# Kernel tuning notes

Hardware: AMD Instinct MI355X
Metric: run time of the kernel (lower is better)

## Reference

```python
import jax, jax.numpy as jnp
import numpy as np
from jax import lax

RANK = 8
ALPHA = 16.0
SCALING = ALPHA / RANK  # 2.0
C_IN, C_OUT, KH, KW = 128, 256, 3, 3


def setup_inputs() -> dict:
    key = jax.random.key(0)
    k1, k2, k3, k4, k5 = jax.random.split(key, 5)
    x = jax.random.normal(k1, (16, C_IN, 64, 64), dtype=jnp.float32)
    W = jax.random.normal(k2, (C_OUT, C_IN, KH, KW), dtype=jnp.float32) * 0.05
    b = jax.random.normal(k3, (C_OUT,), dtype=jnp.float32) * 0.05
    lora_A = jax.random.normal(k4, (RANK, C_IN * KH * KW), dtype=jnp.float32) * 0.02
    lora_B = jax.random.normal(k5, (C_OUT, RANK), dtype=jnp.float32) * 0.02
    return {"x": x, "W": W, "b": b, "lora_A": lora_A, "lora_B": lora_B}


def _conv(x, w, stride=(1, 1), padding=((1, 1), (1, 1))):
    return lax.conv_general_dilated(
        x, w, window_strides=stride, padding=padding,
        dimension_numbers=("NCHW", "OIHW", "NCHW"))


def reference(x, W, b, lora_A, lora_B):
    # Base (frozen) conv: [B, C_out, H, W]
    base_out = _conv(x, W) + b[None, :, None, None]
    # LoRA path. The torch code does im2col -> (BL, C_in*kh*kw) @ A.T @ B.T.
    # Because unfold flattens patches channel-major as (C_in, kh, kw), the
    # identical math is: rank-r conv with A reshaped as [rank, C_in, kh, kw],
    # then a 1x1 mix with B. Same result, no im2col materialization.
    A_k = lora_A.reshape(RANK, C_IN, KH, KW)
    h = _conv(x, A_k)                                   # [B, rank, H, W]
    lora_out = jnp.einsum("brhw,or->bohw", h, lora_B) * SCALING
    return base_out + lora_out
```

## Files before the change

kernel.cpp:

```cpp
#include <hip/hip_runtime.h>
#include <hip/hip_bf16.h>


#define CIN   128
#define COUT  256
#define NBAT  16
#define HPAD  66
#define WPAD  66

typedef __bf16 bf16x8 __attribute__((ext_vector_type(8)));
typedef float f32x4 __attribute__((ext_vector_type(4)));

#define XPAD_ELEMS ((size_t)NBAT * HPAD * WPAD * CIN)
#define XPAD_BYTES (XPAD_ELEMS * 2)
#define WT_ELEMS   ((size_t)9 * COUT * CIN)
#define WS_NEED    (XPAD_BYTES + WT_ELEMS * 2)

typedef __attribute__((address_space(1))) void gvoid;
typedef __attribute__((address_space(3))) void lvoid;

__device__ __forceinline__ void load_lds16(const void* g, void* l) {
    __builtin_amdgcn_global_load_lds((gvoid*)g, (lvoid*)l, 16, 0, 0);
}

__global__ void pad_prep(const float* __restrict__ x, __bf16* __restrict__ xpad,
                         const float* __restrict__ W, const float* __restrict__ lA,
                         const float* __restrict__ lB, __hip_bfloat16* __restrict__ Wt) {
    __shared__ float tile[128][66];
    const int t = threadIdx.x;

    if (blockIdx.x >= 1024) {
        const int idx = (blockIdx.x - 1024) * 256 + t;
        const int c = idx & 127;
        const int o = idx >> 7;
        const int fr    = o & 15;
        const int otile = o >> 4;
        const int cb    = c >> 5;
        const int kc    = (c >> 3) & 3;
        const int j     = c & 7;
        const int lane  = kc * 16 + fr;
        float lb[8];
#pragma unroll
        for (int r = 0; r < 8; ++r) lb[r] = lB[o * 8 + r];
#pragma unroll
        for (int tap = 0; tap < 9; ++tap) {
            float acc = W[(o * 128 + c) * 9 + tap];
            float s = 0.f;
#pragma unroll
            for (int r = 0; r < 8; ++r)
                s += lb[r] * lA[r * 1152 + c * 9 + tap];
            const size_t widx = (((size_t)(tap * 4 + cb) * 16 + otile) * 64 + lane) * 8 + j;
            Wt[widx] = __float2bfloat16(acc + 2.0f * s);
        }
        return;
    }

    const int n = blockIdx.x >> 6;
    const int h = blockIdx.x & 63;
    const float* src = x + (size_t)n * 128 * 4096 + (size_t)h * 64;
#pragma unroll
    for (int i = 0; i < 8; ++i) {
        int g  = i * 256 + t;
        int c  = g >> 4;
        int w4 = (g & 15) * 4;
        const float4 v = *reinterpret_cast<const float4*>(src + (size_t)c * 4096 + w4);
        const int wb = w4 ^ (((c >> 3) & 7) << 2);
        tile[c][wb + 0] = v.x; tile[c][wb + 1] = v.y;
        tile[c][wb + 2] = v.z; tile[c][wb + 3] = v.w;
    }
    __syncthreads();
    __bf16* dst = xpad + ((size_t)(n * 66 + h + 1) * 66 + 1) * 128;
#pragma unroll
    for (int i = 0; i < 4; ++i) {
        int g  = i * 256 + t;
        int w  = g >> 4;
        int c0 = (g & 15) * 8;
        const int swr = ((c0 >> 3) & 7) << 2;
        bf16x8 v;
#pragma unroll
        for (int j = 0; j < 8; ++j) v[j] = (__bf16)tile[c0 + j][w ^ swr];
        *reinterpret_cast<bf16x8*>(dst + (size_t)w * 128 + c0) = v;
    }
    bf16x8 z = {};
    __bf16* rowbase = xpad + (size_t)(n * 66 + h + 1) * 66 * 128;
    if (t < 32) {
        int ww = (t < 16) ? 0 : 65;
        int c0 = (t & 15) * 8;
        *reinterpret_cast<bf16x8*>(rowbase + (size_t)ww * 128 + c0) = z;
    }
    if (h == 0 || h == 63) {
        __bf16* hrow = xpad + (size_t)(n * 66 + (h == 0 ? 0 : 65)) * 66 * 128;
        for (int i = t; i < 66 * 16; i += 256)
            *reinterpret_cast<bf16x8*>(hrow + (size_t)i * 8) = z;
    }
}

__global__ void __launch_bounds__(512, 2) conv_mfma(
    const __bf16* __restrict__ xpad, const __bf16* __restrict__ Wt,
    const float* __restrict__ bias, float* __restrict__ out) {
    __shared__ __align__(16) __bf16 lds[32768];

    const int tid  = threadIdx.x;
    const int wv   = tid >> 6;
    const int lane = tid & 63;

    const int n  = blockIdx.x >> 4;
    const int h0 = (blockIdx.x & 15) << 2;

    const int lrow = lane >> 2;
    const int lswz = (((lane & 3) ^ ((lane >> 3) & 3)) << 3);
    const __bf16* bG[2];
#pragma unroll
    for (int j = 0; j < 2; ++j) {
        const int r0 = j * 128 + wv * 16;
        bG[j] = xpad + (((size_t)(n * 66 + h0 + (r0 >> 6)) * 66 + (r0 & 63) + lrow) * 128) + lswz;
    }

    const int wo   = (wv >> 2) << 7;
    const int wot  = (wv >> 2) << 3;
    const int wpix = (wv & 3) << 6;
    const int fr   = lane & 15;
    const int fphys = (((lane >> 4) ^ ((lane >> 1) & 3)) << 3);
    const int b_rd = (wpix + fr) * 32 + fphys;

    const __bf16* wG = Wt + (size_t)wot * 512 + lane * 8;

    f32x4 acc[4][8] = {};
    f32x4 wA[8], wB[8];

#define WL(dst, ptr, imm)                                                      \
    asm volatile("global_load_dwordx4 %0, %1, off offset:" #imm                \
                 : "=&v"(dst) : "v"(ptr) : "memory")

#define WLOADS(WN, u) do {                                                     \
        const __bf16* wp0_ = wG + (size_t)(u) * 8192;                          \
        const __bf16* wp1_ = wp0_ + 2048;                                      \
        WL(WN[0], wp0_, 0);    WL(WN[1], wp0_, 1024);                          \
        WL(WN[2], wp0_, 2048); WL(WN[3], wp0_, 3072);                          \
        WL(WN[4], wp1_, 0);    WL(WN[5], wp1_, 1024);                          \
        WL(WN[6], wp1_, 2048); WL(WN[7], wp1_, 3072);                          \
    } while (0)

#define STAGE(u) do {                                                          \
        const int u_ = (u);                                                    \
        const int tap_ = u_ >> 2, cb_ = u_ & 3;                                \
        const int kh_ = (tap_ >= 6) ? 2 : (tap_ >= 3 ? 1 : 0);                 \
        const int kw_ = tap_ - kh_ * 3;                                        \
        const int bo_ = (kh_ * 66 + kw_) * 128 + cb_ * 32;                     \
        const int lb_ = (u_ & 3) * 8192;                                       \
        load_lds16(bG[0] + bo_, lds + lb_ + (wv * 16) * 32);                   \
        load_lds16(bG[1] + bo_, lds + lb_ + (128 + wv * 16) * 32);             \
    } while (0)

#define COMPUTE(t_, WC) do {                                                   \
        const __bf16* Bb = lds + ((t_) & 3) * 8192 + b_rd;                     \
        bf16x8 bfr[4];                                                         \
        _Pragma("unroll")                                                      \
        for (int pi = 0; pi < 4; ++pi)                                         \
            bfr[pi] = *reinterpret_cast<const bf16x8*>(Bb + pi * 512);         \
        __builtin_amdgcn_s_setprio(1);                                         \
        _Pragma("unroll")                                                      \
        for (int pi = 0; pi < 4; ++pi)                                         \
            _Pragma("unroll")                                                  \
            for (int oi = 0; oi < 8; ++oi)                                     \
                acc[pi][oi] = __builtin_amdgcn_mfma_f32_16x16x32_bf16(         \
                    bfr[pi], __builtin_bit_cast(bf16x8, WC[oi]),               \
                    acc[pi][oi], 0, 0, 0);                                     \
        __builtin_amdgcn_s_setprio(0);                                         \
    } while (0)

#define BODY(t_, WC, WN) do {                                                  \
        asm volatile("s_waitcnt vmcnt(2)" ::: "memory");                       \
        __builtin_amdgcn_sched_barrier(0);                                     \
        __builtin_amdgcn_s_barrier();                                          \
        __builtin_amdgcn_sched_barrier(0);                                     \
        WLOADS(WN, (t_) + 1);                                                  \
        __builtin_amdgcn_sched_barrier(0);                                     \
        STAGE((t_) + 2);                                                       \
        __builtin_amdgcn_sched_barrier(0);                                     \
        COMPUTE(t_, WC);                                                       \
    } while (0)

    WLOADS(wA, 0);
    __builtin_amdgcn_sched_barrier(0);
    STAGE(0);
    STAGE(1);
    __builtin_amdgcn_sched_barrier(0);

    for (int tt = 0; tt < 17; ++tt) {
        BODY(2 * tt,     wA, wB);
        BODY(2 * tt + 1, wB, wA);
    }
    asm volatile("s_waitcnt vmcnt(2)" ::: "memory");
    __builtin_amdgcn_sched_barrier(0);
    __builtin_amdgcn_s_barrier();
    __builtin_amdgcn_sched_barrier(0);
    WLOADS(wB, 35);
    __builtin_amdgcn_sched_barrier(0);
    COMPUTE(34, wA);
    asm volatile("s_waitcnt vmcnt(0)" ::: "memory");
    __builtin_amdgcn_sched_barrier(0);
    __builtin_amdgcn_s_barrier();
    __builtin_amdgcn_sched_barrier(0);
    COMPUTE(35, wB);

#undef BODY
#undef COMPUTE
#undef STAGE
#undef WLOADS
#undef WL

    const int col = lane & 15;
    const int q4  = (lane >> 4) << 2;
    const int h   = h0 + (wpix >> 6);
    float bo[8];
#pragma unroll
    for (int oi = 0; oi < 8; ++oi) bo[oi] = bias[wo + oi * 16 + col];
#pragma unroll
    for (int pi = 0; pi < 4; ++pi) {
        const int w0 = pi * 16 + q4;
#pragma unroll
        for (int oi = 0; oi < 8; ++oi) {
            const int o = wo + oi * 16 + col;
            f32x4 v;
#pragma unroll
            for (int j = 0; j < 4; ++j) v[j] = acc[pi][oi][j] + bo[oi];
            *reinterpret_cast<f32x4*>(out + (((size_t)n * 256 + o) * 64 + h) * 64 + w0) = v;
        }
    }
}

__global__ void conv_naive(const float* __restrict__ x, const float* __restrict__ W,
                           const float* __restrict__ b, const float* __restrict__ lA,
                           const float* __restrict__ lB, float* __restrict__ out) {
    int idx = blockIdx.x * 256 + threadIdx.x;
    int w = idx & 63, h = (idx >> 6) & 63, o = (idx >> 12) & 255, n = idx >> 20;
    float acc = b[o];
    float hr[8] = {0, 0, 0, 0, 0, 0, 0, 0};
    for (int c = 0; c < 128; ++c)
        for (int kh = 0; kh < 3; ++kh) {
            int hy = h + kh - 1;
            if (hy < 0 || hy > 63) continue;
            for (int kw = 0; kw < 3; ++kw) {
                int wx = w + kw - 1;
                if (wx < 0 || wx > 63) continue;
                float xv = x[((n * 128 + c) * 64 + hy) * 64 + wx];
                int ka = c * 9 + kh * 3 + kw;
                acc += W[(o * 128 + c) * 9 + kh * 3 + kw] * xv;
#pragma unroll
                for (int r = 0; r < 8; ++r) hr[r] += lA[r * 1152 + ka] * xv;
            }
        }
    float ls = 0.f;
#pragma unroll
    for (int r = 0; r < 8; ++r) ls += lB[o * 8 + r] * hr[r];
    out[idx] = acc + 2.0f * ls;
}

extern "C" void kernel_launch(void* const* d_in, const int* in_sizes, int n_in,
                              void* d_out, int out_size, void* d_ws, size_t ws_size,
                              hipStream_t stream) {
    const float* x  = (const float*)d_in[0];
    const float* W  = (const float*)d_in[1];
    const float* b  = (const float*)d_in[2];
    const float* lA = (const float*)d_in[3];
    const float* lB = (const float*)d_in[4];
    float* out = (float*)d_out;

    if (ws_size < WS_NEED) {
        conv_naive<<<out_size / 256, 256, 0, stream>>>(x, W, b, lA, lB, out);
        return;
    }

    __bf16* xpad = (__bf16*)d_ws;
    __hip_bfloat16* Wt = (__hip_bfloat16*)((char*)d_ws + XPAD_BYTES);

    pad_prep<<<1024 + 128, 256, 0, stream>>>(x, xpad, W, lA, lB, Wt);
    conv_mfma<<<256, 512, 0, stream>>>(xpad, (const __bf16*)Wt, b, out);
}
```

Before: 136.3 us.

## Retile conv MFMA kernel to 2x4 wave grid with 64-channel K steps

Reorganizes the implicit-GEMM conv kernel so the eight waves form a 2 (pixel) x 4 (output-channel) grid instead of 2x4 transposed ownership, with K steps of 64 channels (18 steps instead of 36). LDS staging doubles to 128KB with four quarter-phases per K step, interleaving LDS fragment reads, staging of step k+2, and MFMAs, with a barrier per phase. The intent is to cut per-step barrier and wait overhead and rebalance LDS versus global weight traffic per wave. The cost is more LDS use, which may limit occupancy to one block per CU despite launch bounds of two, plus many more barriers per step.

```diff
diff --git a/kernel.cpp b/kernel.cpp
--- a/kernel.cpp
+++ b/kernel.cpp
@@ -98,133 +98,150 @@
 __global__ void __launch_bounds__(512, 2) conv_mfma(
     const __bf16* __restrict__ xpad, const __bf16* __restrict__ Wt,
     const float* __restrict__ bias, float* __restrict__ out) {
-    __shared__ __align__(16) __bf16 lds[32768];
+    __shared__ __align__(16) __bf16 lds[65536];
 
     const int tid  = threadIdx.x;
     const int wv   = tid >> 6;
     const int lane = tid & 63;
+    const int wm   = wv >> 2;
+    const int wn   = wv & 3;
 
     const int n  = blockIdx.x >> 4;
     const int h0 = (blockIdx.x & 15) << 2;
 
-    const int lrow = lane >> 2;
-    const int lswz = (((lane & 3) ^ ((lane >> 3) & 3)) << 3);
-    const __bf16* bG[2];
-#pragma unroll
-    for (int j = 0; j < 2; ++j) {
-        const int r0 = j * 128 + wv * 16;
-        bG[j] = xpad + (((size_t)(n * 66 + h0 + (r0 >> 6)) * 66 + (r0 & 63) + lrow) * 128) + lswz;
-    }
-
-    const int wo   = (wv >> 2) << 7;
-    const int wot  = (wv >> 2) << 3;
-    const int wpix = (wv & 3) << 6;
-    const int fr   = lane & 15;
-    const int fphys = (((lane >> 4) ^ ((lane >> 1) & 3)) << 3);
-    const int b_rd = (wpix + fr) * 32 + fphys;
-
-    const __bf16* wG = Wt + (size_t)wot * 512 + lane * 8;
-
-    f32x4 acc[4][8] = {};
+    const __bf16* xq[4];
+#pragma unroll
+    for (int q = 0; q < 4; ++q)
+        xq[q] = xpad + (((size_t)(n * 66 + h0 + q) * 66) + wv * 8 + (lane >> 3)) * 128
+                     + (((lane & 7) ^ (lane >> 3)) << 3);
+
+    const int b_base = (wm * 128 + (lane & 15)) * 64;
+    const int ph0 = (((lane >> 4) ^ (lane & 7)) << 3);
+    const int ph1 = ph0 ^ 32;
+
+    const __bf16* wGbase = Wt + (size_t)(wn * 4) * 512 + lane * 8;
+
+    f32x4 acc[8][4] = {};
     f32x4 wA[8], wB[8];
 
 #define WL(dst, ptr, imm)                                                      \
     asm volatile("global_load_dwordx4 %0, %1, off offset:" #imm                \
                  : "=&v"(dst) : "v"(ptr) : "memory")
 
-#define WLOADS(WN, u) do {                                                     \
-        const __bf16* wp0_ = wG + (size_t)(u) * 8192;                          \
-        const __bf16* wp1_ = wp0_ + 2048;                                      \
-        WL(WN[0], wp0_, 0);    WL(WN[1], wp0_, 1024);                          \
-        WL(WN[2], wp0_, 2048); WL(WN[3], wp0_, 3072);                          \
-        WL(WN[4], wp1_, 0);    WL(WN[5], wp1_, 1024);                          \
-        WL(WN[6], wp1_, 2048); WL(WN[7], wp1_, 3072);                          \
-    } while (0)
-
-#define STAGE(u) do {                                                          \
-        const int u_ = (u);                                                    \
-        const int tap_ = u_ >> 2, cb_ = u_ & 3;                                \
+#define WLOADS(WN, u_) do {                                                    \
+        const int tap_ = (u_) >> 1, ch_ = (u_) & 1;                            \
+        const __bf16* w0_ = wGbase + (size_t)(tap_ * 4 + ch_ * 2) * 8192;      \
+        const __bf16* w1_ = w0_ + 8192;                                        \
+        WL(WN[0], w0_, 0);    WL(WN[1], w0_, 1024);                            \
+        WL(WN[2], w0_, 2048); WL(WN[3], w0_, 3072);                            \
+        WL(WN[4], w1_, 0);    WL(WN[5], w1_, 1024);                            \
+        WL(WN[6], w1_, 2048); WL(WN[7], w1_, 3072);                            \
+    } while (0)
+
+#define STAGEQ(u_, q_) do {                                                    \
+        const int tap_ = (u_) >> 1, ch_ = (u_) & 1;                            \
         const int kh_ = (tap_ >= 6) ? 2 : (tap_ >= 3 ? 1 : 0);                 \
         const int kw_ = tap_ - kh_ * 3;                                        \
-        const int bo_ = (kh_ * 66 + kw_) * 128 + cb_ * 32;                     \
-        const int lb_ = (u_ & 3) * 8192;                                       \
-        load_lds16(bG[0] + bo_, lds + lb_ + (wv * 16) * 32);                   \
-        load_lds16(bG[1] + bo_, lds + lb_ + (128 + wv * 16) * 32);             \
-    } while (0)
-
-#define COMPUTE(t_, WC) do {                                                   \
-        const __bf16* Bb = lds + ((t_) & 3) * 8192 + b_rd;                     \
-        bf16x8 bfr[4];                                                         \
-        _Pragma("unroll")                                                      \
-        for (int pi = 0; pi < 4; ++pi)                                         \
-            bfr[pi] = *reinterpret_cast<const bf16x8*>(Bb + pi * 512);         \
+        const int off_ = (kh_ * 66 + kw_) * 128 + ch_ * 64;                    \
+        load_lds16(xq[q_] + off_,                                              \
+                   lds + ((u_) & 3) * 16384 + (q_) * 4096 + wv * 512);         \
+    } while (0)
+
+#define MF(P, KS, AI, OJ)                                                      \
+    acc[AI][OJ] = __builtin_amdgcn_mfma_f32_16x16x32_bf16(                     \
+        P, __builtin_bit_cast(bf16x8, WC[(KS) * 4 + (OJ)]), acc[AI][OJ], 0, 0, 0)
+
+#define PHASE(kt_, q_, WCp, DO_STAGE) do {                                     \
+        const f32x4* const WC = (WCp);                                         \
+        const __bf16* Pb_ = lds + ((kt_) & 3) * 16384 + b_base                 \
+                          + ((q_) >> 1) * 4096;                                \
+        bf16x8 p00 = *(const bf16x8*)(Pb_ + ph0);                              \
+        bf16x8 p01 = *(const bf16x8*)(Pb_ + ph1);                              \
+        bf16x8 p10 = *(const bf16x8*)(Pb_ + 1024 + ph0);                       \
+        bf16x8 p11 = *(const bf16x8*)(Pb_ + 1024 + ph1);                       \
+        if (DO_STAGE) STAGEQ((kt_) + 2, q_);                                   \
+        __builtin_amdgcn_s_barrier();                                          \
         __builtin_amdgcn_s_setprio(1);                                         \
-        _Pragma("unroll")                                                      \
-        for (int pi = 0; pi < 4; ++pi)                                         \
-            _Pragma("unroll")                                                  \
-            for (int oi = 0; oi < 8; ++oi)                                     \
-                acc[pi][oi] = __builtin_amdgcn_mfma_f32_16x16x32_bf16(         \
-                    bfr[pi], __builtin_bit_cast(bf16x8, WC[oi]),               \
-                    acc[pi][oi], 0, 0, 0);                                     \
+        MF(p00, 0, ((q_) >> 1) * 4 + 0, ((q_) & 1) * 2 + 0);                   \
+        MF(p00, 0, ((q_) >> 1) * 4 + 0, ((q_) & 1) * 2 + 1);                   \
+        MF(p01, 1, ((q_) >> 1) * 4 + 0, ((q_) & 1) * 2 + 0);                   \
+        MF(p01, 1, ((q_) >> 1) * 4 + 0, ((q_) & 1) * 2 + 1);                   \
+        MF(p10, 0, ((q_) >> 1) * 4 + 1, ((q_) & 1) * 2 + 0);                   \
+        MF(p10, 0, ((q_) >> 1) * 4 + 1, ((q_) & 1) * 2 + 1);                   \
+        MF(p11, 1, ((q_) >> 1) * 4 + 1, ((q_) & 1) * 2 + 0);                   \
+        MF(p11, 1, ((q_) >> 1) * 4 + 1, ((q_) & 1) * 2 + 1);                   \
         __builtin_amdgcn_s_setprio(0);                                         \
-    } while (0)
-
-#define BODY(t_, WC, WN) do {                                                  \
-        asm volatile("s_waitcnt vmcnt(2)" ::: "memory");                       \
+        bf16x8 p20 = *(const bf16x8*)(Pb_ + 2048 + ph0);                       \
+        bf16x8 p21 = *(const bf16x8*)(Pb_ + 2048 + ph1);                       \
+        bf16x8 p30 = *(const bf16x8*)(Pb_ + 3072 + ph0);                       \
+        bf16x8 p31 = *(const bf16x8*)(Pb_ + 3072 + ph1);                       \
+        __builtin_amdgcn_s_setprio(1);                                         \
+        MF(p20, 0, ((q_) >> 1) * 4 + 2, ((q_) & 1) * 2 + 0);                   \
+        MF(p20, 0, ((q_) >> 1) * 4 + 2, ((q_) & 1) * 2 + 1);                   \
+        MF(p21, 1, ((q_) >> 1) * 4 + 2, ((q_) & 1) * 2 + 0);                   \
+        MF(p21, 1, ((q_) >> 1) * 4 + 2, ((q_) & 1) * 2 + 1);                   \
+        MF(p30, 0, ((q_) >> 1) * 4 + 3, ((q_) & 1) * 2 + 0);                   \
+        MF(p30, 0, ((q_) >> 1) * 4 + 3, ((q_) & 1) * 2 + 1);                   \
+        MF(p31, 1, ((q_) >> 1) * 4 + 3, ((q_) & 1) * 2 + 0);                   \
+        MF(p31, 1, ((q_) >> 1) * 4 + 3, ((q_) & 1) * 2 + 1);                   \
+        __builtin_amdgcn_s_setprio(0);                                         \
+    } while (0)
+
+#define KTBODY(kt_, WCk, WN) do {                                              \
+        WLOADS(WN, (kt_) + 1);                                                 \
+        PHASE(kt_, 0, WCk, 1); PHASE(kt_, 1, WCk, 1);                          \
+        PHASE(kt_, 2, WCk, 1); PHASE(kt_, 3, WCk, 1);                          \
+        asm volatile("s_waitcnt vmcnt(4)" ::: "memory");                       \
         __builtin_amdgcn_sched_barrier(0);                                     \
         __builtin_amdgcn_s_barrier();                                          \
         __builtin_amdgcn_sched_barrier(0);                                     \
-        WLOADS(WN, (t_) + 1);                                                  \
-        __builtin_amdgcn_sched_barrier(0);                                     \
-        STAGE((t_) + 2);                                                       \
-        __builtin_amdgcn_sched_barrier(0);                                     \
-        COMPUTE(t_, WC);                                                       \
     } while (0)
 
     WLOADS(wA, 0);
-    __builtin_amdgcn_sched_barrier(0);
-    STAGE(0);
-    STAGE(1);
-    __builtin_amdgcn_sched_barrier(0);
-
-    for (int tt = 0; tt < 17; ++tt) {
-        BODY(2 * tt,     wA, wB);
-        BODY(2 * tt + 1, wB, wA);
-    }
-    asm volatile("s_waitcnt vmcnt(2)" ::: "memory");
+    STAGEQ(0, 0); STAGEQ(0, 1); STAGEQ(0, 2); STAGEQ(0, 3);
+    STAGEQ(1, 0); STAGEQ(1, 1); STAGEQ(1, 2); STAGEQ(1, 3);
+    asm volatile("s_waitcnt vmcnt(4)" ::: "memory");
     __builtin_amdgcn_sched_barrier(0);
     __builtin_amdgcn_s_barrier();
     __builtin_amdgcn_sched_barrier(0);
-    WLOADS(wB, 35);
-    __builtin_amdgcn_sched_barrier(0);
-    COMPUTE(34, wA);
+
+    for (int ktt = 0; ktt < 8; ++ktt) {
+        KTBODY(2 * ktt,     wA, wB);
+        KTBODY(2 * ktt + 1, wB, wA);
+    }
+    WLOADS(wB, 17);
+    PHASE(16, 0, wA, 0); PHASE(16, 1, wA, 0);
+    PHASE(16, 2, wA, 0); PHASE(16, 3, wA, 0);
     asm volatile("s_waitcnt vmcnt(0)" ::: "memory");
     __builtin_amdgcn_sched_barrier(0);
     __builtin_amdgcn_s_barrier();
     __builtin_amdgcn_sched_barrier(0);
-    COMPUTE(35, wB);
-
-#undef BODY
-#undef COMPUTE
-#undef STAGE
+    PHASE(17, 0, wB, 0); PHASE(17, 1, wB, 0);
+    PHASE(17, 2, wB, 0); PHASE(17, 3, wB, 0);
+
+#undef KTBODY
+#undef PHASE
+#undef MF
+#undef STAGEQ
 #undef WLOADS
 #undef WL
 
     const int col = lane & 15;
     const int q4  = (lane >> 4) << 2;
-    const int h   = h0 + (wpix >> 6);
-    float bo[8];
-#pragma unroll
-    for (int oi = 0; oi < 8; ++oi) bo[oi] = bias[wo + oi * 16 + col];
-#pragma unroll
-    for (int pi = 0; pi < 4; ++pi) {
-        const int w0 = pi * 16 + q4;
-#pragma unroll
-        for (int oi = 0; oi < 8; ++oi) {
-            const int o = wo + oi * 16 + col;
+    float bo[4];
+#pragma unroll
+    for (int oj = 0; oj < 4; ++oj) bo[oj] = bias[wn * 64 + oj * 16 + col];
+#pragma unroll
+    for (int pi = 0; pi < 8; ++pi) {
+        const int X  = pi * 16 + q4;
+        const int h  = h0 + wm * 2 + (X >> 6);
+        const int w0 = X & 63;
+#pragma unroll
+        for (int oj = 0; oj < 4; ++oj) {
+            const int o = wn * 64 + oj * 16 + col;
             f32x4 v;
 #pragma unroll
-            for (int j = 0; j < 4; ++j) v[j] = acc[pi][oi][j] + bo[oi];
+            for (int j = 0; j < 4; ++j) v[j] = acc[pi][oj][j] + bo[oj];
             *reinterpret_cast<f32x4*>(out + (((size_t)n * 256 + o) * 64 + h) * 64 + w0) = v;
         }
     }
```

Measured after the change: 141.3 us. 1.04x slower.
